# Kernel tuning notes

Measured on AMD Instinct MI355X. Metric: run time of the kernel, lower is better.

Reference implementation:

```python
import jax, jax.numpy as jnp
import numpy as np

CLIP = 100000.0
T, N, C, H, E = 8, 1024, 64, 256, 32768
NC = N * (N + 1) // 2


def _ntn(t):
    return jnp.nan_to_num(t, nan=0.0, posinf=CLIP, neginf=-CLIP)


def _gcn_conv(x, row, col, ew, W, b, n):
    # PyG GCNConv: sym-normalized aggregation (self-loops already appended)
    h = x @ W  # [n, out]
    deg = jax.ops.segment_sum(ew, col, num_segments=n)
    dinv = jnp.where(deg > 0, jax.lax.rsqrt(jnp.where(deg > 0, deg, 1.0)), 0.0)
    norm = dinv[row] * ew * dinv[col]  # [e]
    out = jax.ops.segment_sum(norm[:, None] * h[row], col, num_segments=n)
    return out + b


def setup_inputs() -> dict:
    key = jax.random.key(0)
    ks = jax.random.split(key, 10)
    return {
        "xs": jax.random.normal(ks[0], (T, N, C), jnp.float32),
        "edge_index": jax.random.randint(ks[1], (T, 2, E), 0, N),
        "edge_weight": jax.random.uniform(ks[2], (T, E), jnp.float32),
        "conv1_w": jax.random.normal(ks[3], (C, H), jnp.float32) * 0.05,
        "conv1_b": jnp.zeros((H,), jnp.float32),
        "conv2_w": jax.random.normal(ks[4], (H, H), jnp.float32) * 0.05,
        "conv2_b": jnp.zeros((H,), jnp.float32),
        "w_ih": jax.random.normal(ks[5], (4 * H, H), jnp.float32) * 0.05,
        "w_hh": jax.random.normal(ks[6], (4 * H, H), jnp.float32) * 0.05,
        "b_ih": jnp.zeros((4 * H,), jnp.float32),
        "b_hh": jnp.zeros((4 * H,), jnp.float32),
        "fc_w": jax.random.normal(ks[7], (H, NC), jnp.float32) * 0.02,
        "fc_b": jnp.zeros((NC,), jnp.float32),
    }


def reference(xs, edge_index, edge_weight, conv1_w, conv1_b, conv2_w, conv2_b,
              w_ih, w_hh, b_ih, b_hh, fc_w, fc_b):
    n = xs.shape[1]
    self_idx = jnp.arange(n)

    def per_step(x, ei, ew):
        # add self-loops with weight 1 (GCNConv default)
        row = jnp.concatenate([ei[0], self_idx])
        col = jnp.concatenate([ei[1], self_idx])
        w = jnp.concatenate([ew, jnp.ones((n,), ew.dtype)])
        h = jax.nn.relu(_ntn(_gcn_conv(x, row, col, w, conv1_w, conv1_b, n)))
        h = jax.nn.relu(_ntn(_gcn_conv(h, row, col, w, conv2_w, conv2_b, n)))
        return _ntn(h.mean(axis=0))  # global mean pool, single graph

    embs = _ntn(jax.vmap(per_step)(xs, edge_index, edge_weight))  # [T, H]

    def lstm_step(carry, x_t):
        h, c = carry
        g = x_t @ w_ih.T + b_ih + h @ w_hh.T + b_hh
        i, f, gg, o = jnp.split(g, 4)
        c = jax.nn.sigmoid(f) * c + jax.nn.sigmoid(i) * jnp.tanh(gg)
        h = jax.nn.sigmoid(o) * jnp.tanh(c)
        return (h, c), h

    hdim = w_hh.shape[1]
    init = (jnp.zeros((hdim,), embs.dtype), jnp.zeros((hdim,), embs.dtype))
    _, hs = jax.lax.scan(lstm_step, init, embs)
    final_h = _ntn(_ntn(hs)[-1])  # [H]

    vec = _ntn(final_h @ fc_w + fc_b)  # [N(N+1)/2]
    tril = jnp.tril_indices(n)  # row-major (i, j<=i) matches torch loop
    L = jnp.zeros((n, n), vec.dtype).at[tril].set(vec)
    return _ntn(L @ L.T)
```

## Files before the change

kernel.cpp:

```cpp
#include <hip/hip_runtime.h>
#include <hip/hip_bf16.h>
#include <math.h>

#define T_ 8
#define N_ 1024
#define C_ 64
#define H_ 256
#define E_ 32768
#define NC_ 524800
#define SLACK 96
#define CLIPV 100000.0f

__device__ __forceinline__ float sigmoidf_(float x) { return 1.0f / (1.0f + __expf(-x)); }

__global__ void scatter_direct_kernel(const int* __restrict__ ei, const float* __restrict__ ew,
                                      float* __restrict__ deg, int* __restrict__ cnt,
                                      int* __restrict__ csr_src, float* __restrict__ csr_ew) {
    int g = blockIdx.x * 256 + threadIdx.x;
    int t = g >> 15, e = g & (E_ - 1);
    int row = ei[t * 2 * E_ + e];
    int col = ei[t * 2 * E_ + E_ + e];
    float w = ew[g];
    int bin = t * N_ + col;
    atomicAdd(&deg[bin], w);
    int pos = atomicAdd(&cnt[bin], 1);
    if (pos < SLACK) {
        csr_src[bin * SLACK + pos] = row;
        csr_ew[bin * SLACK + pos] = w;
    }
}

__global__ __launch_bounds__(256) void sgemm_nn(const float* __restrict__ A,
                                                const float* __restrict__ B,
                                                float* __restrict__ C,
                                                int M, int N, int K) {
    __shared__ float As[16][68];
    __shared__ float Bs[16][68];
    int tid = threadIdx.x;
    int tx = tid & 15, ty = tid >> 4;
    int m0 = blockIdx.y * 64, n0 = blockIdx.x * 64;
    float acc[4][4] = {{0.f}};
    for (int k0 = 0; k0 < K; k0 += 16) {
        int ka = tid & 15, ma = tid >> 4;
#pragma unroll
        for (int mm = 0; mm < 64; mm += 16)
            As[ka][ma + mm] = A[(size_t)(m0 + ma + mm) * K + k0 + ka];
        int nb = tid & 63, kb = tid >> 6;
#pragma unroll
        for (int kk = 0; kk < 16; kk += 4)
            Bs[kb + kk][nb] = B[(size_t)(k0 + kb + kk) * N + n0 + nb];
        __syncthreads();
#pragma unroll
        for (int kk = 0; kk < 16; ++kk) {
            float4 a4 = *(const float4*)&As[kk][ty * 4];
            float4 b4 = *(const float4*)&Bs[kk][tx * 4];
            float a[4] = {a4.x, a4.y, a4.z, a4.w};
            float b[4] = {b4.x, b4.y, b4.z, b4.w};
#pragma unroll
            for (int i = 0; i < 4; ++i)
#pragma unroll
                for (int j = 0; j < 4; ++j) acc[i][j] += a[i] * b[j];
        }
        __syncthreads();
    }
#pragma unroll
    for (int i = 0; i < 4; ++i) {
        float4 o = make_float4(acc[i][0], acc[i][1], acc[i][2], acc[i][3]);
        *(float4*)&C[(size_t)(m0 + ty * 4 + i) * N + n0 + tx * 4] = o;
    }
}

template <bool POOL>
__global__ __launch_bounds__(256) void agg_kernel(const float* __restrict__ hin,
                                                  const float* __restrict__ deg,
                                                  const int* __restrict__ cnt,
                                                  const int* __restrict__ csr_src,
                                                  const float* __restrict__ csr_ew,
                                                  const float* __restrict__ bias,
                                                  float* __restrict__ out) {
    __shared__ int s_src[SLACK];
    __shared__ float s_nrm[SLACK];
    int bx = blockIdx.x;
    int t = bx >> 10, j = bx & 1023;
    int c = threadIdx.x;
    float dj = rsqrtf(deg[bx] + 1.0f);
    int count = min(cnt[bx], SLACK);
    const float* hbase = hin + (size_t)(t * N_) * H_;
    const float* dbase = deg + t * N_;
    float self = hin[(size_t)bx * H_ + c];
    if (c < count) {
        int s = csr_src[bx * SLACK + c];
        s_src[c] = s;
        s_nrm[c] = csr_ew[bx * SLACK + c] * rsqrtf(dbase[s] + 1.0f);
    }
    __syncthreads();
    float a0 = 0.f, a1 = 0.f, a2 = 0.f, a3 = 0.f;
    int u = 0;
    for (; u + 3 < count; u += 4) {
        int s0 = s_src[u], s1 = s_src[u + 1], s2 = s_src[u + 2], s3 = s_src[u + 3];
        float n0 = s_nrm[u], n1 = s_nrm[u + 1], n2 = s_nrm[u + 2], n3 = s_nrm[u + 3];
        a0 += n0 * hbase[(size_t)s0 * H_ + c];
        a1 += n1 * hbase[(size_t)s1 * H_ + c];
        a2 += n2 * hbase[(size_t)s2 * H_ + c];
        a3 += n3 * hbase[(size_t)s3 * H_ + c];
    }
    for (; u < count; ++u) a0 += s_nrm[u] * hbase[(size_t)s_src[u] * H_ + c];
    float accE = (a0 + a1) + (a2 + a3);
    float val = dj * (dj * self + accE) + bias[c];
    val = fminf(fmaxf(val, 0.0f), CLIPV);
    if (POOL)
        atomicAdd(&out[(size_t)(t * 32 + (j & 31)) * H_ + c], val * (1.0f / 1024.0f));
    else
        out[(size_t)bx * H_ + c] = val;
}

__global__ __launch_bounds__(256) void xg_pool_kernel(const float* __restrict__ pool_part,
                                                      const float* __restrict__ w_ih,
                                                      const float* __restrict__ b_ih,
                                                      const float* __restrict__ b_hh,
                                                      float* __restrict__ xg) {
    __shared__ float s_e[H_];
    int b = blockIdx.x;
    int t = b >> 2;
    int tid = threadIdx.x;
    int j = (b & 3) * 256 + tid;
    float a = 0.f;
#pragma unroll
    for (int g2 = 0; g2 < 32; ++g2) a += pool_part[(size_t)(t * 32 + g2) * H_ + tid];
    s_e[tid] = fminf(fmaxf(a, -CLIPV), CLIPV);
    __syncthreads();
    const float4* wr = (const float4*)(w_ih + (size_t)j * H_);
    float acc = b_ih[j] + b_hh[j];
#pragma unroll 4
    for (int k4 = 0; k4 < H_ / 4; ++k4) {
        float4 w = wr[k4];
        acc += w.x * s_e[k4 * 4] + w.y * s_e[k4 * 4 + 1] + w.z * s_e[k4 * 4 + 2] + w.w * s_e[k4 * 4 + 3];
    }
    xg[t * 1024 + j] = acc;
}

__device__ __forceinline__ void gbar(int* bar, int target) {
    __syncthreads();
    if (threadIdx.x == 0) {
        __threadfence();
        __hip_atomic_fetch_add(bar, 1, __ATOMIC_ACQ_REL, __HIP_MEMORY_SCOPE_AGENT);
        long spin = 0;
        while (__hip_atomic_load(bar, __ATOMIC_ACQUIRE, __HIP_MEMORY_SCOPE_AGENT) < target) {
            if (++spin > (1L << 27)) break;
        }
    }
    __syncthreads();
}

__global__ __launch_bounds__(1024) void lstm_all_kernel(const float* __restrict__ xg,
                                                        const float* __restrict__ w_hh,
                                                        float* __restrict__ gbuf,
                                                        int* __restrict__ bar,
                                                        float* __restrict__ final_h) {
    __shared__ float s_h[H_];
    int tid = threadIdx.x;
    int jl = tid >> 2, q = tid & 3;
    int j = blockIdx.x * 256 + jl;
    float4 wreg[16];
    const float4* wr = (const float4*)(w_hh + (size_t)j * H_ + q * 64);
#pragma unroll
    for (int r = 0; r < 16; ++r) wreg[r] = wr[r];
    float c_reg = 0.f;
    for (int s = 0; s < T_; ++s) {
        if (s == 0) {
            if (tid < 256) s_h[tid] = 0.f;
        } else {
            if (tid < 256) {
                const float* gp = gbuf + ((s - 1) & 1) * 1024;
                float gi = gp[tid], gf = gp[256 + tid], gg = gp[512 + tid], go = gp[768 + tid];
                c_reg = sigmoidf_(gf) * c_reg + sigmoidf_(gi) * tanhf(gg);
                s_h[tid] = sigmoidf_(go) * tanhf(c_reg);
            }
        }
        __syncthreads();
        float acc = 0.f;
#pragma unroll
        for (int r = 0; r < 16; ++r) {
            float4 w = wreg[r];
            int k = q * 64 + r * 4;
            acc += w.x * s_h[k] + w.y * s_h[k + 1] + w.z * s_h[k + 2] + w.w * s_h[k + 3];
        }
        acc += __shfl_xor(acc, 1);
        acc += __shfl_xor(acc, 2);
        if (q == 0) gbuf[(s & 1) * 1024 + j] = xg[s * 1024 + j] + acc;
        gbar(bar, 4 * (s + 1));
    }
    if (blockIdx.x == 0 && tid < 256) {
        const float* gp = gbuf + ((T_ - 1) & 1) * 1024;
        float gi = gp[tid], gf = gp[256 + tid], gg = gp[512 + tid], go = gp[768 + tid];
        float cc = sigmoidf_(gf) * c_reg + sigmoidf_(gi) * tanhf(gg);
        final_h[tid] = sigmoidf_(go) * tanhf(cc);
    }
}

__device__ __forceinline__ void store_quad(float4 v, int j0, float* __restrict__ Lm) {
    int i = (int)((sqrtf(8.0f * (float)j0 + 1.0f) - 1.0f) * 0.5f);
    while ((i + 1) * (i + 2) / 2 <= j0) ++i;
    while (i * (i + 1) / 2 > j0) --i;
    int rb = i * (i + 1) / 2, col = j0 - rb;
    if (col + 3 <= i) {
        *(float4*)&Lm[(size_t)i * 1024 + col] = v;
    } else {
        float vv[4] = {v.x, v.y, v.z, v.w};
#pragma unroll
        for (int e = 0; e < 4; ++e) {
            int jj = j0 + e;
            while ((i + 1) * (i + 2) / 2 <= jj) ++i;
            Lm[(size_t)i * 1024 + (jj - i * (i + 1) / 2)] = vv[e];
        }
    }
}

__global__ __launch_bounds__(256) void fc_kernel(const float* __restrict__ final_h,
                                                 const float* __restrict__ fc_w,
                                                 const float* __restrict__ fc_b,
                                                 float* __restrict__ Lm) {
    __shared__ float s_h[H_];
    __shared__ float4 s_red[256];
    int tid = threadIdx.x;
    s_h[tid] = final_h[tid];
    __syncthreads();
    const int NQ = NC_ / 4;
    int lane = tid & 63, grp = tid >> 6;
    int j4 = blockIdx.x * 64 + lane;
    const float4* w4 = (const float4*)fc_w;
    float4 acc = make_float4(0.f, 0.f, 0.f, 0.f);
    int k0 = grp * 64;
#pragma unroll 8
    for (int i = 0; i < 64; ++i) {
        int k = k0 + i;
        float4 w = w4[(size_t)k * NQ + j4];
        float hk = s_h[k];
        acc.x += hk * w.x; acc.y += hk * w.y; acc.z += hk * w.z; acc.w += hk * w.w;
    }
    s_red[tid] = acc;
    __syncthreads();
    if (tid < 64) {
        float4 a0 = s_red[tid], a1 = s_red[64 + tid], a2 = s_red[128 + tid], a3 = s_red[192 + tid];
        float4 b = ((const float4*)fc_b)[j4];
        float4 r;
        r.x = a0.x + a1.x + a2.x + a3.x + b.x;
        r.y = a0.y + a1.y + a2.y + a3.y + b.y;
        r.z = a0.z + a1.z + a2.z + a3.z + b.z;
        r.w = a0.w + a1.w + a2.w + a3.w + b.w;
        r.x = fminf(fmaxf(r.x, -CLIPV), CLIPV);
        r.y = fminf(fmaxf(r.y, -CLIPV), CLIPV);
        r.z = fminf(fmaxf(r.z, -CLIPV), CLIPV);
        r.w = fminf(fmaxf(r.w, -CLIPV), CLIPV);
        store_quad(r, j4 * 4, Lm);
    }
}

__global__ __launch_bounds__(256) void syrk_kernel(const float* __restrict__ L, float* __restrict__ Cout) {
    int b = blockIdx.x;
    int I = (int)((sqrtf(8.0f * b + 1.0f) - 1.0f) * 0.5f);
    while ((I + 1) * (I + 2) / 2 <= b) ++I;
    while (I * (I + 1) / 2 > b) --I;
    int J = b - I * (I + 1) / 2;
    int Klim = (J + 1) * 64;
    int kbeg = blockIdx.y * 256;
    int kend = min(Klim, kbeg + 256);
    if (kbeg >= kend) return;

    __shared__ float As[16][68];
    __shared__ float Bs[16][68];
    int tid = threadIdx.x;
    int tx = tid & 15, ty = tid >> 4;
    int m0 = I * 64, n0 = J * 64;
    float acc[4][4] = {{0.f}};
    for (int k0 = kbeg; k0 < kend; k0 += 16) {
        int ka = tid & 15, ma = tid >> 4;
#pragma unroll
        for (int mm = 0; mm < 64; mm += 16) {
            As[ka][ma + mm] = L[(size_t)(m0 + ma + mm) * 1024 + k0 + ka];
            Bs[ka][ma + mm] = L[(size_t)(n0 + ma + mm) * 1024 + k0 + ka];
        }
        __syncthreads();
#pragma unroll
        for (int kk = 0; kk < 16; ++kk) {
            float4 a4 = *(const float4*)&As[kk][ty * 4];
            float4 b4 = *(const float4*)&Bs[kk][tx * 4];
            float a[4] = {a4.x, a4.y, a4.z, a4.w};
            float bb[4] = {b4.x, b4.y, b4.z, b4.w};
#pragma unroll
            for (int i = 0; i < 4; ++i)
#pragma unroll
                for (int j = 0; j < 4; ++j) acc[i][j] += a[i] * bb[j];
        }
        __syncthreads();
    }
#pragma unroll
    for (int i = 0; i < 4; ++i)
#pragma unroll
        for (int j = 0; j < 4; ++j)
            atomicAdd(&Cout[(size_t)(m0 + ty * 4 + i) * 1024 + n0 + tx * 4 + j], acc[i][j]);
}

__global__ __launch_bounds__(256) void mirror_kernel(float* __restrict__ Cout) {
    int J = blockIdx.x, I = blockIdx.y;
    if (J >= I) return;
    __shared__ float s[64][65];
    int cc = threadIdx.x & 63, r0 = threadIdx.x >> 6;
    for (int r = r0; r < 64; r += 4)
        s[r][cc] = Cout[(size_t)(I * 64 + r) * 1024 + J * 64 + cc];
    __syncthreads();
    for (int r = r0; r < 64; r += 4)
        Cout[(size_t)(J * 64 + r) * 1024 + I * 64 + cc] = s[cc][r];
}

extern "C" void kernel_launch(void* const* d_in, const int* in_sizes, int n_in,
                              void* d_out, int out_size, void* d_ws, size_t ws_size,
                              hipStream_t stream) {
    const float* xs      = (const float*)d_in[0];
    const int*   ei      = (const int*)d_in[1];
    const float* ew      = (const float*)d_in[2];
    const float* conv1_w = (const float*)d_in[3];
    const float* conv1_b = (const float*)d_in[4];
    const float* conv2_w = (const float*)d_in[5];
    const float* conv2_b = (const float*)d_in[6];
    const float* w_ih    = (const float*)d_in[7];
    const float* w_hh    = (const float*)d_in[8];
    const float* b_ih    = (const float*)d_in[9];
    const float* b_hh    = (const float*)d_in[10];
    const float* fc_w    = (const float*)d_in[11];
    const float* fc_b    = (const float*)d_in[12];
    float* out = (float*)d_out;

    float* ws = (float*)d_ws;
    size_t off = 0;
    float* xw1  = ws + off; off += (size_t)T_ * N_ * H_;
    float* h1   = ws + off; off += (size_t)T_ * N_ * H_;
    float* Lm   = ws + off; off += (size_t)N_ * N_;
    float* deg  = ws + off; off += T_ * N_;
    int*   cnt  = (int*)(ws + off); off += T_ * N_;
    float* pool_part = ws + off; off += T_ * 32 * H_;
    int*   bar  = (int*)(ws + off); off += 256;
    size_t zero_bytes = ((size_t)N_ * N_ + (size_t)(T_ * N_) * 2 + T_ * 32 * H_ + 256) * 4;
    float* zero_base = Lm;
    float* csr_ew = ws + off; off += (size_t)T_ * N_ * SLACK;
    float* xg   = ws + off; off += T_ * 4 * H_;
    float* gbuf = ws + off; off += 2 * 1024;
    float* final_h = ws + off; off += 256;
    int* csr_src = (int*)(ws + off); off += (size_t)T_ * N_ * SLACK;
    (void)ws_size; (void)in_sizes; (void)n_in; (void)out_size;

    hipMemsetAsync(zero_base, 0, zero_bytes, stream);
    hipMemsetAsync(out, 0, (size_t)N_ * N_ * sizeof(float), stream);

    scatter_direct_kernel<<<(T_ * E_) / 256, 256, 0, stream>>>(ei, ew, deg, cnt, csr_src, csr_ew);

    sgemm_nn<<<dim3(H_ / 64, (T_ * N_) / 64), 256, 0, stream>>>(xs, conv1_w, xw1, T_ * N_, H_, C_);
    agg_kernel<false><<<T_ * N_, 256, 0, stream>>>(xw1, deg, cnt, csr_src, csr_ew, conv1_b, h1);
    sgemm_nn<<<dim3(H_ / 64, (T_ * N_) / 64), 256, 0, stream>>>(h1, conv2_w, xw1, T_ * N_, H_, H_);
    agg_kernel<true><<<T_ * N_, 256, 0, stream>>>(xw1, deg, cnt, csr_src, csr_ew, conv2_b, pool_part);

    xg_pool_kernel<<<32, 256, 0, stream>>>(pool_part, w_ih, b_ih, b_hh, xg);
    lstm_all_kernel<<<4, 1024, 0, stream>>>(xg, w_hh, gbuf, bar, final_h);

    fc_kernel<<<NC_ / 4 / 64, 256, 0, stream>>>(final_h, fc_w, fc_b, Lm);

    syrk_kernel<<<dim3(136, 4), 256, 0, stream>>>(Lm, out);
    mirror_kernel<<<dim3(16, 16), 256, 0, stream>>>(out);
}
```

Baseline: 307.8 us.

## Fuse SYRK with mirror store, drop output memset and atomics, pack CSR

```diff
diff --git a/kernel.cpp b/kernel.cpp
--- a/kernel.cpp
+++ b/kernel.cpp
@@ -13,9 +13,14 @@
 
 __device__ __forceinline__ float sigmoidf_(float x) { return 1.0f / (1.0f + __expf(-x)); }
 
+__global__ void zero_init_kernel(float* base, int n) {
+    int g = blockIdx.x * 256 + threadIdx.x;
+    if (g < n) base[g] = 0.0f;
+}
+
 __global__ void scatter_direct_kernel(const int* __restrict__ ei, const float* __restrict__ ew,
                                       float* __restrict__ deg, int* __restrict__ cnt,
-                                      int* __restrict__ csr_src, float* __restrict__ csr_ew) {
+                                      int2* __restrict__ csr) {
     int g = blockIdx.x * 256 + threadIdx.x;
     int t = g >> 15, e = g & (E_ - 1);
     int row = ei[t * 2 * E_ + e];
@@ -25,8 +30,8 @@
     atomicAdd(&deg[bin], w);
     int pos = atomicAdd(&cnt[bin], 1);
     if (pos < SLACK) {
-        csr_src[bin * SLACK + pos] = row;
-        csr_ew[bin * SLACK + pos] = w;
+        int2 v; v.x = row; v.y = __float_as_int(w);
+        csr[bin * SLACK + pos] = v;
     }
 }
 
@@ -74,8 +79,7 @@
 __global__ __launch_bounds__(256) void agg_kernel(const float* __restrict__ hin,
                                                   const float* __restrict__ deg,
                                                   const int* __restrict__ cnt,
-                                                  const int* __restrict__ csr_src,
-                                                  const float* __restrict__ csr_ew,
+                                                  const int2* __restrict__ csr,
                                                   const float* __restrict__ bias,
                                                   float* __restrict__ out) {
     __shared__ int s_src[SLACK];
@@ -89,9 +93,9 @@
     const float* dbase = deg + t * N_;
     float self = hin[(size_t)bx * H_ + c];
     if (c < count) {
-        int s = csr_src[bx * SLACK + c];
-        s_src[c] = s;
-        s_nrm[c] = csr_ew[bx * SLACK + c] * rsqrtf(dbase[s] + 1.0f);
+        int2 v = csr[bx * SLACK + c];
+        s_src[c] = v.x;
+        s_nrm[c] = __int_as_float(v.y) * rsqrtf(dbase[v.x] + 1.0f);
     }
     __syncthreads();
     float a0 = 0.f, a1 = 0.f, a2 = 0.f, a3 = 0.f;
@@ -256,61 +260,63 @@
     }
 }
 
-__global__ __launch_bounds__(256) void syrk_kernel(const float* __restrict__ L, float* __restrict__ Cout) {
+__global__ __launch_bounds__(512) void syrk_fused_kernel(const float* __restrict__ L,
+                                                         float* __restrict__ Cout) {
+    __shared__ float As[16][68];
+    __shared__ float Bs[16][68];
+    __shared__ float tr[64][65];
     int b = blockIdx.x;
     int I = (int)((sqrtf(8.0f * b + 1.0f) - 1.0f) * 0.5f);
     while ((I + 1) * (I + 2) / 2 <= b) ++I;
     while (I * (I + 1) / 2 > b) --I;
     int J = b - I * (I + 1) / 2;
     int Klim = (J + 1) * 64;
-    int kbeg = blockIdx.y * 256;
-    int kend = min(Klim, kbeg + 256);
-    if (kbeg >= kend) return;
-
-    __shared__ float As[16][68];
-    __shared__ float Bs[16][68];
-    int tid = threadIdx.x;
-    int tx = tid & 15, ty = tid >> 4;
     int m0 = I * 64, n0 = J * 64;
-    float acc[4][4] = {{0.f}};
-    for (int k0 = kbeg; k0 < kend; k0 += 16) {
-        int ka = tid & 15, ma = tid >> 4;
-#pragma unroll
-        for (int mm = 0; mm < 64; mm += 16) {
-            As[ka][ma + mm] = L[(size_t)(m0 + ma + mm) * 1024 + k0 + ka];
-            Bs[ka][ma + mm] = L[(size_t)(n0 + ma + mm) * 1024 + k0 + ka];
+    int tid = threadIdx.x;
+    int tx = tid & 31, ty = tid >> 5;
+    float acc[4][2] = {{0.f}};
+    int ka = tid & 15, ma0 = tid >> 4;
+    for (int k0 = 0; k0 < Klim; k0 += 16) {
+#pragma unroll
+        for (int mm = 0; mm < 64; mm += 32) {
+            int rA = m0 + ma0 + mm, rB = n0 + ma0 + mm, kg = k0 + ka;
+            float va = L[(size_t)rA * 1024 + kg];
+            float vb = L[(size_t)rB * 1024 + kg];
+            As[ka][ma0 + mm] = (kg <= rA) ? va : 0.f;
+            Bs[ka][ma0 + mm] = (kg <= rB) ? vb : 0.f;
         }
         __syncthreads();
 #pragma unroll
         for (int kk = 0; kk < 16; ++kk) {
             float4 a4 = *(const float4*)&As[kk][ty * 4];
-            float4 b4 = *(const float4*)&Bs[kk][tx * 4];
+            float2 b2 = *(const float2*)&Bs[kk][tx * 2];
             float a[4] = {a4.x, a4.y, a4.z, a4.w};
-            float bb[4] = {b4.x, b4.y, b4.z, b4.w};
-#pragma unroll
-            for (int i = 0; i < 4; ++i)
-#pragma unroll
-                for (int j = 0; j < 4; ++j) acc[i][j] += a[i] * bb[j];
-        }
-        __syncthreads();
-    }
-#pragma unroll
-    for (int i = 0; i < 4; ++i)
-#pragma unroll
-        for (int j = 0; j < 4; ++j)
-            atomicAdd(&Cout[(size_t)(m0 + ty * 4 + i) * 1024 + n0 + tx * 4 + j], acc[i][j]);
-}
-
-__global__ __launch_bounds__(256) void mirror_kernel(float* __restrict__ Cout) {
-    int J = blockIdx.x, I = blockIdx.y;
-    if (J >= I) return;
-    __shared__ float s[64][65];
-    int cc = threadIdx.x & 63, r0 = threadIdx.x >> 6;
-    for (int r = r0; r < 64; r += 4)
-        s[r][cc] = Cout[(size_t)(I * 64 + r) * 1024 + J * 64 + cc];
-    __syncthreads();
-    for (int r = r0; r < 64; r += 4)
-        Cout[(size_t)(J * 64 + r) * 1024 + I * 64 + cc] = s[cc][r];
+#pragma unroll
+            for (int i = 0; i < 4; ++i) {
+                acc[i][0] += a[i] * b2.x;
+                acc[i][1] += a[i] * b2.y;
+            }
+        }
+        __syncthreads();
+    }
+#pragma unroll
+    for (int i = 0; i < 4; ++i) {
+        float2 o = make_float2(acc[i][0], acc[i][1]);
+        *(float2*)&Cout[(size_t)(m0 + ty * 4 + i) * 1024 + n0 + tx * 2] = o;
+    }
+    if (I != J) {
+#pragma unroll
+        for (int i = 0; i < 4; ++i) {
+            tr[ty * 4 + i][tx * 2] = acc[i][0];
+            tr[ty * 4 + i][tx * 2 + 1] = acc[i][1];
+        }
+        __syncthreads();
+        for (int q = tid; q < 1024; q += 512) {
+            int r = q >> 4, c4 = (q & 15) * 4;
+            float4 v = make_float4(tr[c4][r], tr[c4 + 1][r], tr[c4 + 2][r], tr[c4 + 3][r]);
+            *(float4*)&Cout[(size_t)(n0 + r) * 1024 + m0 + c4] = v;
+        }
+    }
 }
 
 extern "C" void kernel_launch(void* const* d_in, const int* in_sizes, int n_in,
@@ -340,30 +346,26 @@
     int*   cnt  = (int*)(ws + off); off += T_ * N_;
     float* pool_part = ws + off; off += T_ * 32 * H_;
     int*   bar  = (int*)(ws + off); off += 256;
-    size_t zero_bytes = ((size_t)N_ * N_ + (size_t)(T_ * N_) * 2 + T_ * 32 * H_ + 256) * 4;
-    float* zero_base = Lm;
-    float* csr_ew = ws + off; off += (size_t)T_ * N_ * SLACK;
+    int zero_elems = T_ * N_ * 2 + T_ * 32 * H_ + 256;
+    float* zero_base = deg;
     float* xg   = ws + off; off += T_ * 4 * H_;
     float* gbuf = ws + off; off += 2 * 1024;
     float* final_h = ws + off; off += 256;
-    int* csr_src = (int*)(ws + off); off += (size_t)T_ * N_ * SLACK;
+    int2* csr = (int2*)(ws + off); off += (size_t)T_ * N_ * SLACK * 2;
     (void)ws_size; (void)in_sizes; (void)n_in; (void)out_size;
 
-    hipMemsetAsync(zero_base, 0, zero_bytes, stream);
-    hipMemsetAsync(out, 0, (size_t)N_ * N_ * sizeof(float), stream);
-
-    scatter_direct_kernel<<<(T_ * E_) / 256, 256, 0, stream>>>(ei, ew, deg, cnt, csr_src, csr_ew);
+    zero_init_kernel<<<(zero_elems + 255) / 256, 256, 0, stream>>>(zero_base, zero_elems);
+    scatter_direct_kernel<<<(T_ * E_) / 256, 256, 0, stream>>>(ei, ew, deg, cnt, csr);
 
     sgemm_nn<<<dim3(H_ / 64, (T_ * N_) / 64), 256, 0, stream>>>(xs, conv1_w, xw1, T_ * N_, H_, C_);
-    agg_kernel<false><<<T_ * N_, 256, 0, stream>>>(xw1, deg, cnt, csr_src, csr_ew, conv1_b, h1);
+    agg_kernel<false><<<T_ * N_, 256, 0, stream>>>(xw1, deg, cnt, csr, conv1_b, h1);
     sgemm_nn<<<dim3(H_ / 64, (T_ * N_) / 64), 256, 0, stream>>>(h1, conv2_w, xw1, T_ * N_, H_, H_);
-    agg_kernel<true><<<T_ * N_, 256, 0, stream>>>(xw1, deg, cnt, csr_src, csr_ew, conv2_b, pool_part);
+    agg_kernel<true><<<T_ * N_, 256, 0, stream>>>(xw1, deg, cnt, csr, conv2_b, pool_part);
 
     xg_pool_kernel<<<32, 256, 0, stream>>>(pool_part, w_ih, b_ih, b_hh, xg);
     lstm_all_kernel<<<4, 1024, 0, stream>>>(xg, w_hh, gbuf, bar, final_h);
 
     fc_kernel<<<NC_ / 4 / 64, 256, 0, stream>>>(final_h, fc_w, fc_b, Lm);
 
-    syrk_kernel<<<dim3(136, 4), 256, 0, stream>>>(Lm, out);
-    mirror_kernel<<<dim3(16, 16), 256, 0, stream>>>(out);
-}
+    syrk_fused_kernel<<<136, 512, 0, stream>>>(Lm, out);
+}
```

Result: slower. 335.8 us (+9.1%).
